# Kernel tuning notes

Hardware: AMD Instinct MI355X
Metric: run time of the kernel (lower is better)

Reference implementation:

```python
import jax, jax.numpy as jnp
import numpy as np
import math
from jax import lax

# db8 decomposition low-pass filter (pywt wavelet.dec_lo), 16 taps
DEC_LO = np.array([-0.00011747678400228192, 0.0006754494059985568,
    -0.0003917403729959771, -0.00487035299301066, 0.008746094047015655,
    0.013981027917015516, -0.04408825393106472, -0.01736930100202211,
    0.128747426620186, 0.00047248457399797254, -0.2840155429624281,
    -0.015829105256023893, 0.5853546836548691, 0.6756307362980128,
    0.3128715909144659, 0.05441584224308161], dtype=np.float64)
BAND_LEN = 16
HALF = 8
REC_LO = DEC_LO[::-1]                              # reconstruction low-pass
REC_HI = DEC_LO * ((-1.0) ** np.arange(BAND_LEN))  # reconstruction high-pass (QMF)


def _band_matrices(size):
    """WaveCNet-style banded DWT matrices for one axis of length `size`.
    Returns (low, high): low (size//2, size), high (size - size//2, size)."""
    s2 = size // 2
    m_lo = np.zeros((s2, size + BAND_LEN - 2))
    m_hi = np.zeros((size - s2, size + BAND_LEN - 2))
    for i in range(s2):
        m_lo[i, 2 * i:2 * i + BAND_LEN] = REC_LO
    for i in range(size - s2):
        m_hi[i, 2 * i:2 * i + BAND_LEN] = REC_HI
    m_lo = m_lo[:, HALF - 1:-(HALF - 1)]
    m_hi = m_hi[:, HALF - 1:-(HALF - 1)]
    return jnp.asarray(m_lo, jnp.float32), jnp.asarray(m_hi, jnp.float32)


def dwt2d(x):
    # x: (..., H, W) -> LL, LH, HL, HH each (..., H//2, W//2)
    H, W = x.shape[-2], x.shape[-1]
    lo0, hi0 = _band_matrices(H)          # (H2,H), (H-H2,H)
    lo1, hi1 = _band_matrices(W)          # (W2,W), (W-W2,W)
    lo1, hi1 = lo1.T, hi1.T               # (W,W2)
    Lp = jnp.matmul(lo0, x)
    Hp = jnp.matmul(hi0, x)
    return Lp @ lo1, Lp @ hi1, Hp @ lo1, Hp @ hi1


def idwt2d(LL, LH, HL, HH):
    H = LL.shape[-2] + HH.shape[-2]
    W = LL.shape[-1] + HH.shape[-1]
    lo0, hi0 = _band_matrices(H)          # (H2,H)
    lo1, hi1 = _band_matrices(W)          # (W2,W)
    L = LL @ lo1 + LH @ hi1               # (...,H2,W)
    Hh = HL @ lo1 + HH @ hi1
    return jnp.matmul(lo0.T, L) + jnp.matmul(hi0.T, Hh)


def inception(x, ws, bs):
    # x: (BN,1,h,w); 6 convs k=1..11, stack + mean
    outs = []
    for i, (w, b) in enumerate(zip(ws, bs)):
        y = lax.conv_general_dilated(x, w, (1, 1), [(i, i), (i, i)],
                dimension_numbers=('NCHW', 'OIHW', 'NCHW')) + b.reshape(1, -1, 1, 1)
        outs.append(y)
    return jnp.mean(jnp.stack(outs, -1), -1)


def median_low(x):
    # torch.median on even-length dim returns the lower middle element
    n = x.shape[-1]
    return jnp.sort(x, axis=-1)[..., (n - 1) // 2][..., None]


def setup_inputs() -> dict:
    key = jax.random.key(0)
    ks = jax.random.split(key, 16)
    B, T, N, D = 8, 128, 100, 256
    inp = {
        'x': jax.random.normal(ks[0], (B, T, N, D), jnp.float32),
        'adj': jax.random.uniform(ks[1], (N, N), jnp.float32),
    }
    for i in range(6):
        k = 2 * i + 1
        std = math.sqrt(2.0 / (k * k))  # kaiming fan_out, out_channels=1
        inp[f'w{i}'] = jax.random.normal(ks[2 + i], (1, 1, k, k), jnp.float32) * std
        inp[f'b{i}'] = jnp.zeros((1,), jnp.float32)
    inp['out_w'] = jax.random.normal(ks[10], (D, D), jnp.float32) / math.sqrt(D)
    inp['out_b'] = jnp.zeros((D,), jnp.float32)
    return inp


def reference(x, adj, w0, w1, w2, w3, w4, w5, b0, b1, b2, b3, b4, b5, out_w, out_b):
    ws = [w0, w1, w2, w3, w4, w5]
    bs = [b0, b1, b2, b3, b4, b5]
    B, T, N, D = x.shape
    dwt_level = 3
    # (B,T,N,D) -> (B*N,1,T,D)
    xd = jnp.transpose(x, (0, 2, 1, 3)).reshape(-1, T, D)[:, None, :, :]
    s2logT = math.sqrt(2.0 * math.log(T))
    LLd, LHd, HLd, HHd = {}, {}, {}, {}
    LL = xd
    for i in range(dwt_level):
        LL, LH, HL, HH = dwt2d(LL)
        thr = median_low(jnp.abs(HH)) / 0.6745 * s2logT  # (BN,1,h,1)
        soft = lambda v: jnp.sign(v) * jnp.maximum(jnp.abs(v) - thr, 0.0)
        LL = inception(LL, ws, bs)
        LLd[i] = LL
        LHd[i] = inception(soft(LH), ws, bs)
        HLd[i] = inception(soft(HL), ws, bs)
        HHd[i] = inception(soft(HH), ws, bs)
    # multi-level reconstruction (deepest first)
    LL = LLd[dwt_level - 1]
    for i in range(dwt_level):
        j = dwt_level - 1 - i
        LL = idwt2d(LL, LHd[j], HLd[j], HHd[j])
    # (BN,1,T,D) -> (BN,T,1,D) -> linear -> (B,T,N,D)
    y = jnp.transpose(LL, (0, 2, 1, 3))
    y = y @ out_w.T + out_b
    y = y[:, :, 0, :].reshape(B, N, T, D)
    return jnp.transpose(y, (0, 2, 1, 3))
```

## Files before the change

kernel.cpp:

```cpp
#include <hip/hip_runtime.h>
#include <math.h>

#define NIMG 800
#define T_DIM 128
#define N_DIM 100
#define D_DIM 256

typedef unsigned short ushort_t;
typedef unsigned int uint_t;
typedef __attribute__((ext_vector_type(8))) short short8;
typedef __attribute__((ext_vector_type(4))) float f32x4;

__constant__ float c_RL[16] = {
     0.05441584224308161,   0.3128715909144659,    0.6756307362980128,    0.5853546836548691,
    -0.015829105256023893, -0.2840155429624281,    0.00047248457399797254,0.128747426620186,
    -0.01736930100202211,  -0.04408825393106472,   0.013981027917015516,  0.008746094047015655,
    -0.00487035299301066,  -0.0003917403729959771, 0.0006754494059985568, -0.00011747678400228192
};
__constant__ float c_RH[16] = {
    -0.00011747678400228192,-0.0006754494059985568,-0.0003917403729959771, 0.00487035299301066,
     0.008746094047015655,  -0.013981027917015516, -0.04408825393106472,   0.01736930100202211,
     0.128747426620186,     -0.00047248457399797254,-0.2840155429624281,   0.015829105256023893,
     0.5853546836548691,    -0.6756307362980128,    0.3128715909144659,   -0.05441584224308161
};

__device__ inline ushort_t f2bf(float f) {
    uint_t u = __float_as_uint(f);
    uint_t r = (u + 0x7FFFu + ((u >> 16) & 1u)) >> 16;
    return (ushort_t)r;
}

__device__ inline float softthr(float x, float th) {
    float m = fabsf(x) - th;
    return (m > 0.f) ? copysignf(m, x) : 0.f;
}

__global__ void k_build_comb(const float* w0, const float* w1, const float* w2,
                             const float* w3, const float* w4, const float* w5,
                             const float* b0, const float* b1, const float* b2,
                             const float* b3, const float* b4, const float* b5,
                             float* comb)
{
    int t = threadIdx.x;
    const float* wp[6] = {w0, w1, w2, w3, w4, w5};
    if (t < 121) {
        int dy = t / 11 - 5, dx = t % 11 - 5;
        int ay = dy < 0 ? -dy : dy, ax = dx < 0 ? -dx : dx;
        int a = ay > ax ? ay : ax;
        float s = 0.f;
        for (int i = a; i < 6; ++i) {
            int k = 2 * i + 1;
            s += wp[i][(i + dy) * k + (i + dx)];
        }
        comb[t] = s * (1.0f / 6.0f);
    } else if (t == 121) {
        comb[121] = (b0[0] + b1[0] + b2[0] + b3[0] + b4[0] + b5[0]) * (1.0f / 6.0f);
    }
}

__global__ void k_cvt_bf16(const float* __restrict__ in, ushort_t* __restrict__ out, int n)
{
    int i = blockIdx.x * blockDim.x + threadIdx.x;
    if (i < n) out[i] = f2bf(in[i]);
}

__global__ __launch_bounds__(256) void k_dwt2d_v3(const float* __restrict__ in,
    float* __restrict__ LL, float* __restrict__ LH,
    float* __restrict__ HL, float* __restrict__ HH,
    int H, int W, int nrb, int nstrips, int level0)
{
    __shared__ float xs[46 * 80];
    __shared__ float LpB[2 * 672];
    __shared__ float HpB[2 * 672];
    int h = H >> 1, w = W >> 1;
    int cpx = gridDim.x >> 3;
    int b0i = blockIdx.x;
    int bid = (b0i & 7) * cpx + (b0i >> 3);
    int per = nrb * nstrips;
    int img = bid / per;
    int rem = bid - img * per;
    int rb = rem / nstrips;
    int q = rem - rb * nstrips;
    int r0 = rb * 16, q0 = q * 32;
    int cb = 2 * q0 - 8;
    int jbase = 2 * r0 - 7;
    int tid = threadIdx.x;

    const float* ip; long rstride;
    if (level0) {
        int bb = img / 100, nn = img - bb * 100;
        ip = in + (long)bb * (T_DIM * N_DIM * D_DIM) + (long)nn * D_DIM;
        rstride = (long)N_DIM * D_DIM;
    } else {
        ip = in + (long)img * H * W;
        rstride = W;
    }

    for (int s = tid; s < 46 * 40; s += 256) {
        int jl = s / 40, k = s - jl * 40;
        int gj = jbase + jl, gc = cb + 2 * k;
        float2 v = make_float2(0.f, 0.f);
        if (gj >= 0 && gj < H && gc >= 0 && gc < W)
            v = *(const float2*)&ip[(long)gj * rstride + gc];
        *(float2*)&xs[jl * 80 + 2 * k] = v;
    }
    __syncthreads();

    for (int s = tid; s < 320; s += 256) {
        int g = s / 80, c = s - g * 80;
        float xv[22];
        const float* bp = xs + (8 * g) * 80 + c;
        #pragma unroll
        for (int k = 0; k < 22; ++k) xv[k] = bp[k * 80];
        #pragma unroll
        for (int o = 0; o < 4; ++o) {
            float sl = 0.f, sh = 0.f;
            #pragma unroll
            for (int t = 0; t < 16; ++t) {
                float v = xv[2 * o + t];
                sl = fmaf(c_RL[t], v, sl);
                sh = fmaf(c_RH[t], v, sh);
            }
            int il = 4 * g + o;
            int a = (c & 1) * 672 + il * 41 + (c >> 1);
            LpB[a] = sl;
            HpB[a] = sh;
        }
    }
    __syncthreads();

    {
        int rl = tid >> 4;
        int cp = tid & 15;
        int cl = cp * 2;
        float Lp0[10], Lp1[10], Hp0[10], Hp1[10];
        int base = rl * 41 + cl;
        #pragma unroll
        for (int k = 0; k < 10; ++k) {
            Lp0[k] = LpB[base + k];
            Lp1[k] = LpB[672 + base + k];
            Hp0[k] = HpB[base + k];
            Hp1[k] = HpB[672 + base + k];
        }
        float rll[2], rlh[2], rhl[2], rhh[2];
        #pragma unroll
        for (int n = 0; n < 2; ++n) {
            float ll = 0.f, lh = 0.f, hl = 0.f, hh = 0.f;
            #pragma unroll
            for (int t = 0; t < 16; ++t) {
                const int p = (t + 1) & 1;
                const int k = n + ((t + 1) >> 1);
                float av = p ? Lp1[k] : Lp0[k];
                float bv = p ? Hp1[k] : Hp0[k];
                ll = fmaf(c_RL[t], av, ll);
                lh = fmaf(c_RH[t], av, lh);
                hl = fmaf(c_RL[t], bv, hl);
                hh = fmaf(c_RH[t], bv, hh);
            }
            rll[n] = ll; rlh[n] = lh; rhl[n] = hl; rhh[n] = hh;
        }
        long o = (long)img * h * w + (long)(r0 + rl) * w + (q0 + cl);
        *(float2*)&LL[o] = make_float2(rll[0], rll[1]);
        *(float2*)&LH[o] = make_float2(rlh[0], rlh[1]);
        *(float2*)&HL[o] = make_float2(rhl[0], rhl[1]);
        *(float2*)&HH[o] = make_float2(rhh[0], rhh[1]);
    }
}

__global__ __launch_bounds__(256) void k_idwt2d_v4(const float* __restrict__ LLp,
    const float* __restrict__ LHp, const float* __restrict__ HLp,
    const float* __restrict__ HHp, float* __restrict__ outp,
    ushort_t* __restrict__ outbf, int H, int W, int nrb, int nstrips, int fin)
{
    __shared__ float subf[4][24][41];
    __shared__ float sLm[24 * 64];
    __shared__ float sHm[24 * 64];
    int h = H >> 1, w = W >> 1;
    int cpx = gridDim.x >> 3;
    int b0i = blockIdx.x;
    int bid = (b0i & 7) * cpx + (b0i >> 3);
    int per = nrb * nstrips;
    int img = bid / per;
    int rem = bid - img * per;
    int rb = rem / nstrips;
    int qs = rem - rb * nstrips;
    int j0 = rb * 32, q0 = qs * 64;
    int rbase = (j0 >> 1) - 4;
    int i0 = (q0 >> 1) - 4;
    int tid = threadIdx.x;
    long ibase = (long)img * h * w;

    for (int s = tid; s < 4 * 24 * 20; s += 256) {
        int b = s / 480;
        int r2 = s - b * 480;
        int r = r2 / 20, c2 = r2 - r * 20;
        int gr = rbase + r, gc = i0 + 2 * c2;
        float2 v = make_float2(0.f, 0.f);
        if (gr >= 0 && gr < h && gc >= 0 && gc < w) {
            const float* p = (b == 0) ? LLp : (b == 1) ? LHp : (b == 2) ? HLp : HHp;
            v = *(const float2*)&p[ibase + (long)gr * w + gc];
        }
        subf[b][r][2 * c2]     = v.x;
        subf[b][r][2 * c2 + 1] = v.y;
    }
    __syncthreads();

    for (int s = tid; s < 24 * 16; s += 256) {
        int r = s >> 4;
        int cg = s & 15;
        int lcb = cg * 2;
        float rs[4][10];
        #pragma unroll
        for (int b = 0; b < 4; ++b)
            #pragma unroll
            for (int k = 0; k < 10; ++k)
                rs[b][k] = subf[b][r][lcb + k];
        float accL[4], accH[4];
        #pragma unroll
        for (int n = 0; n < 4; ++n) {
            const int t0 = (n & 1) ? 0 : 1;
            const int kb = ((n & 1) ? 8 : 7) + (n >> 1);
            float aL = 0.f, aH = 0.f;
            #pragma unroll
            for (int tt = 0; tt < 8; ++tt) {
                const int t = t0 + 2 * tt;
                const int k = kb - tt;
                aL = fmaf(c_RL[t], rs[0][k], aL);
                aL = fmaf(c_RH[t], rs[1][k], aL);
                aH = fmaf(c_RL[t], rs[2][k], aH);
                aH = fmaf(c_RH[t], rs[3][k], aH);
            }
            accL[n] = aL; accH[n] = aH;
        }
        *(float4*)&sLm[r * 64 + cg * 4] = make_float4(accL[0], accL[1], accL[2], accL[3]);
        *(float4*)&sHm[r * 64 + cg * 4] = make_float4(accH[0], accH[1], accH[2], accH[3]);
    }
    __syncthreads();

    {
        int g = tid >> 6;
        int cl = tid & 63;
        float rL[12], rH[12];
        #pragma unroll
        for (int k = 0; k < 12; ++k) {
            rL[k] = sLm[(4 * g + k) * 64 + cl];
            rH[k] = sHm[(4 * g + k) * 64 + cl];
        }
        #pragma unroll
        for (int m = 0; m < 8; ++m) {
            const int t0 = (m & 1) ? 0 : 1;
            const int kb = ((m & 1) ? 8 : 7) + (m >> 1);
            float v = 0.f;
            #pragma unroll
            for (int tt = 0; tt < 8; ++tt) {
                const int t = t0 + 2 * tt;
                const int k = kb - tt;
                v = fmaf(c_RL[t], rL[k], v);
                v = fmaf(c_RH[t], rH[k], v);
            }
            int j = j0 + g * 8 + m;
            long o = (long)img * H * W + (long)j * W + q0 + cl;
            if (fin) outbf[o] = f2bf(v);
            else outp[o] = v;
        }
    }
}

template<int W>
__global__ __launch_bounds__(256) void k_med_v2(const float* __restrict__ HH,
    float* __restrict__ thr, float scale)
{
    constexpr int R = 256 / W;
    __shared__ float smv[256];
    int tid = threadIdx.x;
    int l = tid % W;
    long row = (long)blockIdx.x * R + tid / W;
    float v = fabsf(HH[row * W + l]);
    #pragma unroll
    for (int k = 2; k <= W; k <<= 1) {
        #pragma unroll
        for (int j = k >> 1; j > 0; j >>= 1) {
            float pv;
            if (j < 64) {
                pv = __shfl_xor(v, j, 64);
            } else {
                smv[tid] = v;
                __syncthreads();
                pv = smv[tid ^ j];
                __syncthreads();
            }
            bool keepmin = ((l & k) == 0) == ((l & j) == 0);
            v = keepmin ? fminf(v, pv) : fmaxf(v, pv);
        }
    }
    if (l == (W - 1) / 2) thr[row] = v * scale;
}

#define PICK(d) ( (d)==-5 ? f3[0] : (d)==-4 ? f0[0] : (d)==-3 ? f1[0] : \
                  (d)==-2 ? f2[0] : (d)==-1 ? f3[1] : (d)==0  ? f0[1] : \
                  (d)==1  ? f1[1] : (d)==2  ? f2[1] : (d)==3  ? f3[2] : \
                  (d)==4  ? f0[2] : (d)==5  ? f1[2] : (d)==6  ? f2[2] : \
                  (d)==7  ? f3[3] : f0[3] )
__global__ __launch_bounds__(256) void k_incept_v8(const float* __restrict__ bands,
    const float* __restrict__ thrp, const float* __restrict__ comb,
    float* __restrict__ oLL, float* __restrict__ oLH,
    float* __restrict__ oHL, float* __restrict__ oHH)
{
    constexpr int TR = 42;
    constexpr int QP = 37;
    constexpr int AS = TR * QP;
    __shared__ float sm4[4 * AS];

    int cpx = gridDim.x >> 3;
    int b0i = blockIdx.x;
    int bid = (b0i & 7) * cpx + (b0i >> 3);
    int rb = bid & 1;
    int bi = bid >> 1;
    int band = bi & 3;
    int img = bi >> 2;
    long S = (long)NIMG * 64 * 128;
    const float* in = bands + (long)band * S + (long)img * (64 * 128);
    float* outp = (band == 0 ? oLL : band == 1 ? oLH : band == 2 ? oHL : oHH)
                  + (long)img * (64 * 128);
    float tmul = (band == 0) ? 0.f : 1.f;
    const float* trow = thrp + (long)img * 64;
    int r0 = rb * 32;
    int tid = threadIdx.x;

    for (int s = tid; s < TR * 36; s += 256) {
        int r = s / 36, qi = s - r * 36;
        int q = qi - 2;
        int gr = r0 - 5 + r;
        float4 v = make_float4(0.f, 0.f, 0.f, 0.f);
        if (gr >= 0 && gr < 64 && q >= 0 && q < 32) {
            v = *(const float4*)&in[(long)gr * 128 + 4 * q];
            float th = tmul * trow[gr];
            v.x = softthr(v.x, th);
            v.y = softthr(v.y, th);
            v.z = softthr(v.z, th);
            v.w = softthr(v.w, th);
        }
        int a = r * QP + qi;
        sm4[0 * AS + a] = v.x;
        sm4[1 * AS + a] = v.y;
        sm4[2 * AS + a] = v.z;
        sm4[3 * AS + a] = v.w;
    }
    __syncthreads();

    int cq = tid & 31;
    int rg = tid >> 5;
    float cb = comb[121];

    float acc[4][4];
    #pragma unroll
    for (int o = 0; o < 4; ++o)
        #pragma unroll
        for (int n = 0; n < 4; ++n) acc[o][n] = 0.f;

    #pragma unroll
    for (int i = 0; i < 14; ++i) {
        int tr = rg * 4 + i;
        int base = tr * QP + cq + 2;
        float f0[4], f1[3], f2[3], f3[4];
        f3[0] = sm4[3 * AS + base - 2];
        f0[0] = sm4[0 * AS + base - 1];
        f1[0] = sm4[1 * AS + base - 1];
        f2[0] = sm4[2 * AS + base - 1];
        f3[1] = sm4[3 * AS + base - 1];
        f0[1] = sm4[0 * AS + base];
        f1[1] = sm4[1 * AS + base];
        f2[1] = sm4[2 * AS + base];
        f3[2] = sm4[3 * AS + base];
        f0[2] = sm4[0 * AS + base + 1];
        f1[2] = sm4[1 * AS + base + 1];
        f2[2] = sm4[2 * AS + base + 1];
        f3[3] = sm4[3 * AS + base + 1];
        f0[3] = sm4[0 * AS + base + 2];
        #pragma unroll
        for (int ky = 0; ky < 11; ++ky) {
            const int o = i - ky;
            if (o >= 0 && o < 4) {
                #pragma unroll
                for (int kx = 0; kx < 11; ++kx) {
                    float cw = comb[ky * 11 + kx];
                    #pragma unroll
                    for (int n = 0; n < 4; ++n) {
                        const int d = n + kx - 5;
                        acc[o][n] = fmaf(PICK(d), cw, acc[o][n]);
                    }
                }
            }
        }
    }

    #pragma unroll
    for (int o = 0; o < 4; ++o) {
        int oy = r0 + rg * 4 + o;
        float4 st = make_float4(acc[o][0] + cb, acc[o][1] + cb,
                                acc[o][2] + cb, acc[o][3] + cb);
        *(float4*)&outp[(long)oy * 128 + 4 * cq] = st;
    }
}

template<int WT, int BH, int OC, int NC>
__global__ __launch_bounds__(256) void k_incept_v7(const float* __restrict__ bands,
    const float* __restrict__ thrp, const float* __restrict__ comb,
    float* __restrict__ oLL, float* __restrict__ oLH,
    float* __restrict__ oHL, float* __restrict__ oHH)
{
    constexpr int Himg = WT / 2;
    constexpr int NRB = Himg / BH;
    constexpr int LW = WT / 2 + 6;
    constexpr int PITCH = WT / 2 + 7;
    constexpr int TR = BH + 10;
    constexpr int NB = WT / NC;
    __shared__ float smE[TR * PITCH + 1];
    __shared__ float smO[TR * PITCH + 1];

    int bid = blockIdx.x;
    int rb = (NRB > 1) ? (bid % NRB) : 0;
    int bi = (NRB > 1) ? (bid / NRB) : bid;
    int band = bi & 3;
    int img = bi >> 2;
    long S = (long)NIMG * Himg * WT;
    const float* in = bands + (long)band * S + (long)img * Himg * WT;
    float* outp = (band == 0 ? oLL : band == 1 ? oLH : band == 2 ? oHL : oHH)
                  + (long)img * Himg * WT;
    float tmul = (band == 0) ? 0.f : 1.f;
    const float* trow = thrp + (long)img * Himg;
    int r0 = rb * BH;
    int tid = threadIdx.x;

    for (int s = tid; s < TR * LW; s += 256) {
        int r = s / LW, j = s - r * LW;
        int c = j - 3;
        int gr = r0 - 5 + r;
        float2 v = make_float2(0.f, 0.f);
        if (gr >= 0 && gr < Himg && c >= 0 && c < WT / 2) {
            v = *(const float2*)&in[(long)gr * WT + 2 * c];
            float th = tmul * trow[gr];
            v.x = softthr(v.x, th);
            v.y = softthr(v.y, th);
        }
        int a = r * PITCH + ((r >> 2) & 1) + j;
        smE[a] = v.x;
        smO[a] = v.y;
    }
    __syncthreads();

    int cq = tid % NB;
    int rg = tid / NB;
    int x0 = cq * NC;
    float cb = comb[121];

    float acc[OC][NC];
    #pragma unroll
    for (int o = 0; o < OC; ++o)
        #pragma unroll
        for (int n = 0; n < NC; ++n) acc[o][n] = 0.f;

    float bufE[NC / 2 + 5], bufO[NC / 2 + 5];

    #pragma unroll
    for (int i = 0; i < OC + 10; ++i) {
        int tr = rg * OC + i;
        int base = tr * PITCH + ((tr >> 2) & 1) + (x0 >> 1);
        #pragma unroll
        for (int j = 0; j < NC / 2 + 5; ++j) {
            bufE[j] = smE[base + j + 1];
            bufO[j] = smO[base + j];
        }
        #pragma unroll
        for (int ky = 0; ky < 11; ++ky) {
            const int o = i - ky;
            if (o >= 0 && o < OC) {
                #pragma unroll
                for (int kx = 0; kx < 11; ++kx) {
                    float cw = comb[ky * 11 + kx];
                    #pragma unroll
                    for (int n = 0; n < NC; ++n) {
                        const int d = n + kx - 5;
                        float v = ((d & 1) == 0) ? bufE[(d + 4) / 2] : bufO[(d + 5) / 2];
                        acc[o][n] = fmaf(v, cw, acc[o][n]);
                    }
                }
            }
        }
    }

    #pragma unroll
    for (int o = 0; o < OC; ++o) {
        int oy = r0 + rg * OC + o;
        float2 st = make_float2(acc[o][0] + cb, acc[o][1] + cb);
        *(float2*)&outp[(long)oy * WT + x0] = st;
    }
}

__global__ __launch_bounds__(256) void k_gemm_bf16(const ushort_t* __restrict__ A,
    const ushort_t* __restrict__ Bw, const float* __restrict__ bias,
    float* __restrict__ out)
{
    __shared__ uint4 Al4[128 * 8];
    __shared__ uint4 Bl4[128 * 8];
    int m0 = blockIdx.x * 128, n0 = blockIdx.y * 128;
    int tid = threadIdx.x;
    int wid = tid >> 6, lane = tid & 63;
    int wr = wid >> 1, wc = wid & 1;
    f32x4 acc[4][4];
    #pragma unroll
    for (int a = 0; a < 4; ++a)
        #pragma unroll
        for (int b = 0; b < 4; ++b)
            acc[a][b] = (f32x4){0.f, 0.f, 0.f, 0.f};

    const uint4* Ag = (const uint4*)A;
    const uint4* Bg = (const uint4*)Bw;
    int row = tid >> 1, half = tid & 1;

    for (int k0 = 0; k0 < 256; k0 += 64) {
        int gca = ((m0 + row) * 256 + k0 + half * 32) >> 3;
        int gcb = ((n0 + row) * 256 + k0 + half * 32) >> 3;
        #pragma unroll
        for (int q = 0; q < 4; ++q) {
            int c = half * 4 + q;
            int sw = c ^ (row & 7);
            Al4[row * 8 + sw] = Ag[gca + q];
            Bl4[row * 8 + sw] = Bg[gcb + q];
        }
        __syncthreads();
        #pragma unroll
        for (int ks = 0; ks < 2; ++ks) {
            short8 af[4], bfr[4];
            int kc = ks * 4 + (lane >> 4);
            #pragma unroll
            for (int mi = 0; mi < 4; ++mi) {
                int r = wr * 64 + mi * 16 + (lane & 15);
                af[mi] = *(const short8*)&Al4[r * 8 + (kc ^ (r & 7))];
            }
            #pragma unroll
            for (int ni = 0; ni < 4; ++ni) {
                int r = wc * 64 + ni * 16 + (lane & 15);
                bfr[ni] = *(const short8*)&Bl4[r * 8 + (kc ^ (r & 7))];
            }
            #pragma unroll
            for (int mi = 0; mi < 4; ++mi)
                #pragma unroll
                for (int ni = 0; ni < 4; ++ni)
                    acc[mi][ni] = __builtin_amdgcn_mfma_f32_16x16x32_bf16(
                        af[mi], bfr[ni], acc[mi][ni], 0, 0, 0);
        }
        __syncthreads();
    }

    #pragma unroll
    for (int ni = 0; ni < 4; ++ni) {
        int d = n0 + wc * 64 + ni * 16 + (lane & 15);
        float bv = bias[d];
        #pragma unroll
        for (int mi = 0; mi < 4; ++mi) {
            #pragma unroll
            for (int r = 0; r < 4; ++r) {
                int m = m0 + wr * 64 + mi * 16 + (lane >> 4) * 4 + r;
                int img = m >> 7, t = m & 127;
                int bb = img / 100, nn = img - bb * 100;
                long ob = (((long)bb * T_DIM + t) * N_DIM + nn) * D_DIM + d;
                out[ob] = acc[mi][ni][r] + bv;
            }
        }
    }
}

extern "C" void kernel_launch(void* const* d_in, const int* in_sizes, int n_in,
                              void* d_out, int out_size, void* d_ws, size_t ws_size,
                              hipStream_t stream)
{
    const float* x = (const float*)d_in[0];
    const float* w0 = (const float*)d_in[2];  const float* b0 = (const float*)d_in[3];
    const float* w1 = (const float*)d_in[4];  const float* b1 = (const float*)d_in[5];
    const float* w2 = (const float*)d_in[6];  const float* b2 = (const float*)d_in[7];
    const float* w3 = (const float*)d_in[8];  const float* b3 = (const float*)d_in[9];
    const float* w4 = (const float*)d_in[10]; const float* b4 = (const float*)d_in[11];
    const float* w5 = (const float*)d_in[12]; const float* b5 = (const float*)d_in[13];
    const float* out_w = (const float*)d_in[14];
    const float* out_b = (const float*)d_in[15];
    float* ws = (float*)d_ws;
    float* outp = (float*)d_out;

    const long S0 = 6553600, S1 = 1638400, S2 = 409600;
    const long RT = 13107200;

    float* pLH[3] = { ws,               ws + 3 * S0,           ws + 3 * S0 + 3 * S1 };
    float* pHL[3] = { ws + S0,          ws + 3 * S0 + S1,      ws + 3 * S0 + 3 * S1 + S2 };
    float* pHH[3] = { ws + 2 * S0,      ws + 3 * S0 + 2 * S1,  ws + 3 * S0 + 3 * S1 + 2 * S2 };
    float* pLL2 = ws + 3 * S0 + 3 * S1 + 3 * S2;
    float* comb = ws + 3 * S0 + 3 * S1 + 4 * S2;
    float* thr  = comb + 128;
    float* wbf_f = thr + 51200;
    float* LLa  = wbf_f + 32768;
    float* LLb  = LLa + S0;
    float* bufA = LLb + S1;
    float* bufLL = bufA + RT;
    ushort_t* wbf = (ushort_t*)wbf_f;
    ushort_t* Abf = (ushort_t*)bufA;
    float* idwt_out2 = bufLL;
    float* idwt_out1 = bufLL + S2 * 4;
    (void)ws_size; (void)in_sizes; (void)n_in; (void)out_size;

    hipLaunchKernelGGL(k_build_comb, dim3(1), dim3(128), 0, stream,
                       w0, w1, w2, w3, w4, w5, b0, b1, b2, b3, b4, b5, comb);
    hipLaunchKernelGGL(k_cvt_bf16, dim3(256), dim3(256), 0, stream, out_w, wbf, 65536);

    float thr_scale = (float)(sqrt(2.0 * log(128.0)) / 0.6745);

    int Hs[3] = {128, 64, 32}, Ws3[3] = {256, 128, 64};
    const float* curLL = x;
    float* convLLout[3] = { LLa, LLb, pLL2 };

    for (int lev = 0; lev < 3; ++lev) {
        int H = Hs[lev], W = Ws3[lev], h = H >> 1, w = W >> 1;
        long S = (long)NIMG * h * w;
        float* rLL = bufLL;
        float* rLH = bufLL + S;
        float* rHL = bufLL + 2 * S;
        float* rHH = bufLL + 3 * S;
        int nrb = h / 16, nstrips = w / 32;
        if (nrb < 1) nrb = 1;
        if (nstrips < 1) nstrips = 1;
        hipLaunchKernelGGL(k_dwt2d_v3, dim3(NIMG * nrb * nstrips), dim3(256), 0, stream,
                           curLL, rLL, rLH, rHL, rHH,
                           H, W, nrb, nstrips, lev == 0 ? 1 : 0);
        long rows = (long)NIMG * h;
        if (lev == 0) {
            hipLaunchKernelGGL(k_med_v2<128>, dim3((int)(rows / 2)), dim3(256), 0, stream,
                               rHH, thr, thr_scale);
            hipLaunchKernelGGL(k_incept_v8, dim3(NIMG * 4 * 2), dim3(256), 0, stream,
                               rLL, thr, comb, convLLout[lev], pLH[lev], pHL[lev], pHH[lev]);
        } else if (lev == 1) {
            hipLaunchKernelGGL(k_med_v2<64>, dim3((int)(rows / 4)), dim3(256), 0, stream,
                               rHH, thr, thr_scale);
            hipLaunchKernelGGL((k_incept_v7<64, 32, 4, 2>), dim3(NIMG * 4), dim3(256), 0, stream,
                               rLL, thr, comb, convLLout[lev], pLH[lev], pHL[lev], pHH[lev]);
        } else {
            hipLaunchKernelGGL(k_med_v2<32>, dim3((int)(rows / 8)), dim3(256), 0, stream,
                               rHH, thr, thr_scale);
            hipLaunchKernelGGL((k_incept_v7<32, 16, 1, 2>), dim3(NIMG * 4), dim3(256), 0, stream,
                               rLL, thr, comb, convLLout[lev], pLH[lev], pHL[lev], pHH[lev]);
        }
        curLL = convLLout[lev];
    }

    hipLaunchKernelGGL(k_idwt2d_v4, dim3(NIMG * 1 * 1), dim3(256), 0, stream,
                       pLL2, pLH[2], pHL[2], pHH[2], idwt_out2, (ushort_t*)0,
                       32, 64, 1, 1, 0);
    hipLaunchKernelGGL(k_idwt2d_v4, dim3(NIMG * 2 * 2), dim3(256), 0, stream,
                       idwt_out2, pLH[1], pHL[1], pHH[1], idwt_out1, (ushort_t*)0,
                       64, 128, 2, 2, 0);
    hipLaunchKernelGGL(k_idwt2d_v4, dim3(NIMG * 4 * 4), dim3(256), 0, stream,
                       idwt_out1, pLH[0], pHL[0], pHH[0], (float*)0, Abf,
                       128, 256, 4, 4, 1);

    dim3 gg(102400 / 128, 2);
    hipLaunchKernelGGL(k_gemm_bf16, gg, dim3(256), 0, stream, Abf, wbf, out_b, outp);
}
```

Before: 449.3 us.

## Enlarge level-0 inception tile to whole image with 4x8 outputs per thread

The level-0 inception kernel now covers the full 64-row image per block instead of two 32-row halves, so the 5-row halo is loaded once rather than twice. Each thread now computes 4x8 outputs instead of 4x4, which lets each shared-memory operand be reused across more FMAs. Row padding is added to the shared arrays (an extra element every few rows, and 688 instead of 672 in the DWT kernel) to spread bank conflicts. The cost is half as many blocks, a larger shared footprint and higher register pressure, which may lower occupancy.

```diff
diff --git a/kernel.cpp b/kernel.cpp
--- a/kernel.cpp
+++ b/kernel.cpp
@@ -70,8 +70,8 @@
     int H, int W, int nrb, int nstrips, int level0)
 {
     __shared__ float xs[46 * 80];
-    __shared__ float LpB[2 * 672];
-    __shared__ float HpB[2 * 672];
+    __shared__ float LpB[2 * 688];
+    __shared__ float HpB[2 * 688];
     int h = H >> 1, w = W >> 1;
     int cpx = gridDim.x >> 3;
     int b0i = blockIdx.x;
@@ -122,7 +122,7 @@
                 sh = fmaf(c_RH[t], v, sh);
             }
             int il = 4 * g + o;
-            int a = (c & 1) * 672 + il * 41 + (c >> 1);
+            int a = (c & 1) * 688 + il * 41 + (c >> 1);
             LpB[a] = sl;
             HpB[a] = sh;
         }
@@ -138,9 +138,9 @@
         #pragma unroll
         for (int k = 0; k < 10; ++k) {
             Lp0[k] = LpB[base + k];
-            Lp1[k] = LpB[672 + base + k];
+            Lp1[k] = LpB[688 + base + k];
             Hp0[k] = HpB[base + k];
-            Hp1[k] = HpB[672 + base + k];
+            Hp1[k] = HpB[688 + base + k];
         }
         float rll[2], rlh[2], rhl[2], rhh[2];
         #pragma unroll
@@ -296,41 +296,39 @@
     if (l == (W - 1) / 2) thr[row] = v * scale;
 }
 
-#define PICK(d) ( (d)==-5 ? f3[0] : (d)==-4 ? f0[0] : (d)==-3 ? f1[0] : \
-                  (d)==-2 ? f2[0] : (d)==-1 ? f3[1] : (d)==0  ? f0[1] : \
-                  (d)==1  ? f1[1] : (d)==2  ? f2[1] : (d)==3  ? f3[2] : \
-                  (d)==4  ? f0[2] : (d)==5  ? f1[2] : (d)==6  ? f2[2] : \
-                  (d)==7  ? f3[3] : f0[3] )
-__global__ __launch_bounds__(256) void k_incept_v8(const float* __restrict__ bands,
+#define PICK9(d) ( (d)==-5 ? f3[0] : (d)==-4 ? f0[0] : (d)==-3 ? f1[0] : \
+                   (d)==-2 ? f2[0] : (d)==-1 ? f3[1] : (d)==0  ? f0[1] : \
+                   (d)==1  ? f1[1] : (d)==2  ? f2[1] : (d)==3  ? f3[2] : \
+                   (d)==4  ? f0[2] : (d)==5  ? f1[2] : (d)==6  ? f2[2] : \
+                   (d)==7  ? f3[3] : (d)==8  ? f0[3] : (d)==9  ? f1[3] : \
+                   (d)==10 ? f2[3] : (d)==11 ? f3[4] : (d)==12 ? f0[4] : f1[4] )
+__global__ __launch_bounds__(256) void k_incept_v9(const float* __restrict__ bands,
     const float* __restrict__ thrp, const float* __restrict__ comb,
     float* __restrict__ oLL, float* __restrict__ oLH,
     float* __restrict__ oHL, float* __restrict__ oHH)
 {
-    constexpr int TR = 42;
+    constexpr int TR = 74;
     constexpr int QP = 37;
-    constexpr int AS = TR * QP;
+    constexpr int AS = TR * QP + 2;
     __shared__ float sm4[4 * AS];
 
     int cpx = gridDim.x >> 3;
     int b0i = blockIdx.x;
     int bid = (b0i & 7) * cpx + (b0i >> 3);
-    int rb = bid & 1;
-    int bi = bid >> 1;
-    int band = bi & 3;
-    int img = bi >> 2;
+    int band = bid & 3;
+    int img = bid >> 2;
     long S = (long)NIMG * 64 * 128;
     const float* in = bands + (long)band * S + (long)img * (64 * 128);
     float* outp = (band == 0 ? oLL : band == 1 ? oLH : band == 2 ? oHL : oHH)
                   + (long)img * (64 * 128);
     float tmul = (band == 0) ? 0.f : 1.f;
     const float* trow = thrp + (long)img * 64;
-    int r0 = rb * 32;
     int tid = threadIdx.x;
 
     for (int s = tid; s < TR * 36; s += 256) {
         int r = s / 36, qi = s - r * 36;
         int q = qi - 2;
-        int gr = r0 - 5 + r;
+        int gr = r - 5;
         float4 v = make_float4(0.f, 0.f, 0.f, 0.f);
         if (gr >= 0 && gr < 64 && q >= 0 && q < 32) {
             v = *(const float4*)&in[(long)gr * 128 + 4 * q];
@@ -340,7 +338,7 @@
             v.z = softthr(v.z, th);
             v.w = softthr(v.w, th);
         }
-        int a = r * QP + qi;
+        int a = r * QP + ((r >> 2) & 1) + qi;
         sm4[0 * AS + a] = v.x;
         sm4[1 * AS + a] = v.y;
         sm4[2 * AS + a] = v.z;
@@ -348,35 +346,29 @@
     }
     __syncthreads();
 
-    int cq = tid & 31;
-    int rg = tid >> 5;
+    int cg = tid & 15;
+    int rg = tid >> 4;
     float cb = comb[121];
 
-    float acc[4][4];
+    float acc[4][8];
     #pragma unroll
     for (int o = 0; o < 4; ++o)
         #pragma unroll
-        for (int n = 0; n < 4; ++n) acc[o][n] = 0.f;
+        for (int n = 0; n < 8; ++n) acc[o][n] = 0.f;
 
     #pragma unroll
     for (int i = 0; i < 14; ++i) {
         int tr = rg * 4 + i;
-        int base = tr * QP + cq + 2;
-        float f0[4], f1[3], f2[3], f3[4];
-        f3[0] = sm4[3 * AS + base - 2];
-        f0[0] = sm4[0 * AS + base - 1];
-        f1[0] = sm4[1 * AS + base - 1];
-        f2[0] = sm4[2 * AS + base - 1];
-        f3[1] = sm4[3 * AS + base - 1];
-        f0[1] = sm4[0 * AS + base];
-        f1[1] = sm4[1 * AS + base];
-        f2[1] = sm4[2 * AS + base];
-        f3[2] = sm4[3 * AS + base];
-        f0[2] = sm4[0 * AS + base + 1];
-        f1[2] = sm4[1 * AS + base + 1];
-        f2[2] = sm4[2 * AS + base + 1];
-        f3[3] = sm4[3 * AS + base + 1];
-        f0[3] = sm4[0 * AS + base + 2];
+        int B = tr * QP + ((tr >> 2) & 1) + 2 * cg;
+        float f0[5], f1[5], f2[4], f3[5];
+        #pragma unroll
+        for (int j = 0; j < 5; ++j) f3[j] = sm4[3 * AS + B + j];
+        #pragma unroll
+        for (int j = 0; j < 5; ++j) f0[j] = sm4[0 * AS + B + 1 + j];
+        #pragma unroll
+        for (int j = 0; j < 5; ++j) f1[j] = sm4[1 * AS + B + 1 + j];
+        #pragma unroll
+        for (int j = 0; j < 4; ++j) f2[j] = sm4[2 * AS + B + 1 + j];
         #pragma unroll
         for (int ky = 0; ky < 11; ++ky) {
             const int o = i - ky;
@@ -385,9 +377,9 @@
                 for (int kx = 0; kx < 11; ++kx) {
                     float cw = comb[ky * 11 + kx];
                     #pragma unroll
-                    for (int n = 0; n < 4; ++n) {
+                    for (int n = 0; n < 8; ++n) {
                         const int d = n + kx - 5;
-                        acc[o][n] = fmaf(PICK(d), cw, acc[o][n]);
+                        acc[o][n] = fmaf(PICK9(d), cw, acc[o][n]);
                     }
                 }
             }
@@ -396,10 +388,13 @@
 
     #pragma unroll
     for (int o = 0; o < 4; ++o) {
-        int oy = r0 + rg * 4 + o;
-        float4 st = make_float4(acc[o][0] + cb, acc[o][1] + cb,
+        int oy = rg * 4 + o;
+        float4 s0 = make_float4(acc[o][0] + cb, acc[o][1] + cb,
                                 acc[o][2] + cb, acc[o][3] + cb);
-        *(float4*)&outp[(long)oy * 128 + 4 * cq] = st;
+        float4 s1 = make_float4(acc[o][4] + cb, acc[o][5] + cb,
+                                acc[o][6] + cb, acc[o][7] + cb);
+        *(float4*)&outp[(long)oy * 128 + 8 * cg] = s0;
+        *(float4*)&outp[(long)oy * 128 + 8 * cg + 4] = s1;
     }
 }
 
@@ -634,7 +629,7 @@
         if (lev == 0) {
             hipLaunchKernelGGL(k_med_v2<128>, dim3((int)(rows / 2)), dim3(256), 0, stream,
                                rHH, thr, thr_scale);
-            hipLaunchKernelGGL(k_incept_v8, dim3(NIMG * 4 * 2), dim3(256), 0, stream,
+            hipLaunchKernelGGL(k_incept_v9, dim3(NIMG * 4), dim3(256), 0, stream,
                                rLL, thr, comb, convLLout[lev], pLH[lev], pHL[lev], pHH[lev]);
         } else if (lev == 1) {
             hipLaunchKernelGGL(k_med_v2<64>, dim3((int)(rows / 4)), dim3(256), 0, stream,
```

Result: slower. 495.2 us (+10.2%).
